# Performance work log

Hardware: AMD Instinct MI355X
Metric: run time of the kernel (lower is better)

The kernel has to match this reference:

```python
import jax, jax.numpy as jnp
import numpy as np

HEAD_DIM = 256
ROTARY_DIM = 128  # max(2, int(0.5*256) rounded down to even)
HALF_ROT = ROTARY_DIM // 2   # 64
HALF_HEAD = HEAD_DIM // 2    # 128
WAVELENGTH = 10000.0
ROPE_SCALING = 1.0
SOFT_CAP = 50.0
EPS = 1e-6
NQ = 8
NKV = 4
GROUPS = NQ // NKV
NEG_INF = -1e9


def rms_norm(x, scale):
    # keras-hub Gemma RMSNorm: fp32 compute, out = x * rsqrt(mean(x^2)+eps) * (1+scale)
    x32 = x.astype(jnp.float32)
    var = jnp.mean(jnp.square(x32), axis=-1, keepdims=True)
    y = x32 * jax.lax.rsqrt(var + EPS)
    return (y * (1.0 + scale.astype(jnp.float32))).astype(x.dtype)


def l2_norm(x):
    # Gemma4VNorm: pure L2 normalization over head_dim, no learned scale
    x32 = x.astype(jnp.float32)
    ss = jnp.sum(jnp.square(x32), axis=-1, keepdims=True)
    return (x32 * jax.lax.rsqrt(ss + EPS)).astype(x.dtype)


def apply_partial_rope(x):
    # x: [B, S, N, HEAD_DIM]. Partial proportional rotation: only the first
    # HALF_ROT elements of each HALF_HEAD half get rotated. RoPE inverse freqs
    # use denominator_dim = HEAD_DIM (not rotary_dim).
    S = x.shape[1]
    inv_freq = 1.0 / (WAVELENGTH ** (jnp.arange(0, ROTARY_DIM, 2, dtype=jnp.float32) / HEAD_DIM))  # [HALF_ROT]
    pos = jnp.arange(S, dtype=jnp.float32) / ROPE_SCALING
    freq = pos[:, None] * inv_freq[None, :]             # [S, HALF_ROT]
    cos = jnp.cos(freq)[None, :, None, :].astype(x.dtype)
    sin = jnp.sin(freq)[None, :, None, :].astype(x.dtype)
    x1 = x[..., :HALF_HEAD]
    x2 = x[..., HALF_HEAD:]
    x1r, x1n = x1[..., :HALF_ROT], x1[..., HALF_ROT:]
    x2r, x2n = x2[..., :HALF_ROT], x2[..., HALF_ROT:]
    # rotate-half form: [x1r, x2r]*cos + [-x2r, x1r]*sin
    y1r = x1r * cos - x2r * sin
    y2r = x2r * cos + x1r * sin
    return jnp.concatenate([y1r, x1n, y2r, x2n], axis=-1)


def setup_inputs() -> dict:
    key = jax.random.key(0)
    ks = jax.random.split(key, 6)
    B, S, D = 2, 2048, 2048
    x = jax.random.normal(ks[0], (B, S, D), jnp.float32)
    # causal mask [B, S, S]
    attention_mask = jnp.broadcast_to(jnp.tril(jnp.ones((S, S), bool))[None], (B, S, S))
    w_scale = 0.02
    Wq = jax.random.normal(ks[1], (NQ, D, HEAD_DIM), jnp.float32) * w_scale
    Wk = jax.random.normal(ks[2], (NKV, D, HEAD_DIM), jnp.float32) * w_scale
    Wv = jax.random.normal(ks[3], (NKV, D, HEAD_DIM), jnp.float32) * w_scale
    Wo = jax.random.normal(ks[4], (NQ, HEAD_DIM, D), jnp.float32) * w_scale
    q_scale = jnp.zeros((HEAD_DIM,), jnp.float32)
    k_scale = jnp.zeros((HEAD_DIM,), jnp.float32)
    return {"x": x, "attention_mask": attention_mask, "Wq": Wq, "Wk": Wk,
            "Wv": Wv, "Wo": Wo, "q_scale": q_scale, "k_scale": k_scale}


def reference(x, attention_mask, Wq, Wk, Wv, Wo, q_scale, k_scale):
    B, S, D = x.shape
    q = jnp.einsum('btd,ndh->btnh', x, Wq)
    q = apply_partial_rope(rms_norm(q, q_scale))
    k = jnp.einsum('bsd,kdh->bskh', x, Wk)
    k = apply_partial_rope(rms_norm(k, k_scale))
    v = l2_norm(jnp.einsum('bsd,kdh->bskh', x, Wv))
    # grouped-query attention, scaling = 1.0 (Gemma4 relies on QK norm)
    qg = q.reshape(B, S, NKV, GROUPS, HEAD_DIM)
    logits = jnp.einsum('btkgh,bskh->bkgts', qg, k)
    # logit soft cap
    logits = jnp.tanh(logits / SOFT_CAP) * SOFT_CAP
    mask = attention_mask[:, None, None, :, :]
    logits = jnp.where(mask, logits, NEG_INF)
    probs = jax.nn.softmax(logits.astype(jnp.float32), axis=-1).astype(logits.dtype)
    out = jnp.einsum('bkgts,bskh->btkgh', probs, v).reshape(B, S, NQ, HEAD_DIM)
    return jnp.einsum('btnh,nhd->btd', out, Wo)
```

## Files before the change

### kernel.cpp

```cpp
#include <hip/hip_runtime.h>

#define AS1 __attribute__((address_space(1)))
#define AS3 __attribute__((address_space(3)))

typedef __attribute__((ext_vector_type(8))) _Float16 f16x8;
typedef __attribute__((ext_vector_type(4))) float f32x4;

__device__ __forceinline__ unsigned short f2h(float f) {
    union { _Float16 h; unsigned short u; } v; v.h = (_Float16)f; return v.u;
}

__device__ __forceinline__ void gload16(const void* g, void* l) {
    __builtin_amdgcn_global_load_lds((const AS1 unsigned int*)g, (AS3 unsigned int*)l, 16, 0, 0);
}

#define GBAR() __builtin_amdgcn_s_barrier()
#define VM4()  asm volatile("s_waitcnt vmcnt(4)" ::: "memory")
#define VM0()  asm volatile("s_waitcnt vmcnt(0)" ::: "memory")

__global__ __launch_bounds__(256) void k_cvt(const float* __restrict__ src,
                                             unsigned short* __restrict__ dst, int n4) {
    int i = blockIdx.x * 256 + threadIdx.x;
    if (i >= n4) return;
    float4 v = ((const float4*)src)[i];
    ushort4 o;
    o.x = f2h(v.x); o.y = f2h(v.y); o.z = f2h(v.z); o.w = f2h(v.w);
    ((ushort4*)dst)[i] = o;
}

__global__ __launch_bounds__(256) void k_transpose_cvt(const float* __restrict__ src,
                                                       unsigned short* __restrict__ dst,
                                                       int ld_src, int ld_dst,
                                                       long zs_src, long zs_dst) {
    __shared__ float tile[32][33];
    long sb = (long)blockIdx.z * zs_src;
    long db = (long)blockIdx.z * zs_dst;
    int c0 = blockIdx.x * 32, r0 = blockIdx.y * 32;
    int tx = threadIdx.x, ty = threadIdx.y;
#pragma unroll
    for (int i = 0; i < 4; i++)
        tile[ty + i * 8][tx] = src[sb + (long)(r0 + ty + i * 8) * ld_src + c0 + tx];
    __syncthreads();
#pragma unroll
    for (int i = 0; i < 4; i++)
        dst[db + (long)(c0 + ty + i * 8) * ld_dst + r0 + tx] = f2h(tile[tx][ty + i * 8]);
}


template<int BUF, int MIH>
__device__ __forceinline__ void rdA(const unsigned short* SA, int wm, int fr, int g,
                                    f16x8 (&af)[4][2]) {
#pragma unroll
    for (int m = 0; m < 4; m++)
#pragma unroll
        for (int kk = 0; kk < 2; kk++) {
            int pos = wm * 64 + m * 16 + fr;
            af[m][kk] = *(const f16x8*)(SA + BUF * 16384 + MIH * 8192 + pos * 64 +
                                        (((kk * 4 + g) ^ (fr & 7)) << 3));
        }
}

template<int BUF, int NIH>
__device__ __forceinline__ void rdB(const unsigned short* SB, int wn, int fr, int g,
                                    f16x8 (&bf)[2][2]) {
#pragma unroll
    for (int ni2 = 0; ni2 < 2; ni2++)
#pragma unroll
        for (int kk = 0; kk < 2; kk++) {
            int pos = wn * 32 + ni2 * 16 + fr;
            bf[ni2][kk] = *(const f16x8*)(SB + BUF * 16384 + NIH * 8192 + pos * 64 +
                                          (((kk * 4 + g) ^ (fr & 7)) << 3));
        }
}

template<int MIH, int NIH>
__device__ __forceinline__ void mm16(f16x8 (&af)[4][2], f16x8 (&bf)[2][2], f32x4 (&acc)[8][4]) {
    __builtin_amdgcn_s_setprio(1);
#pragma unroll
    for (int m = 0; m < 4; m++)
#pragma unroll
        for (int ni2 = 0; ni2 < 2; ni2++)
#pragma unroll
            for (int kk = 0; kk < 2; kk++)
                acc[MIH * 4 + m][NIH * 2 + ni2] = __builtin_amdgcn_mfma_f32_16x16x32_f16(
                    af[m][kk], bf[ni2][kk], acc[MIH * 4 + m][NIH * 2 + ni2], 0, 0, 0);
    __builtin_amdgcn_s_setprio(0);
}

__global__ __launch_bounds__(512, 1) void k_gemm256(const unsigned short* __restrict__ A,
                                                    const unsigned short* __restrict__ Bt,
                                                    float* __restrict__ C,
                                                    int M, int N, int K, int nbx) {
    __shared__ __align__(16) unsigned short sm[65536];
    unsigned short* SA = sm;
    unsigned short* SB = sm + 32768;

    int tid = threadIdx.x, lane = tid & 63, wid = tid >> 6;
    int g = lane >> 4, fr = lane & 15;
    int wm = wid >> 2, wn = wid & 3;

    int bid = blockIdx.x;
    int sid = (bid & 7) * ((int)gridDim.x >> 3) + (bid >> 3);
    int by = sid / nbx, bx = sid % nbx;
    int rowA0 = by * 256, colB0 = bx * 256;

    f32x4 acc[8][4];
#pragma unroll
    for (int mi = 0; mi < 8; mi++)
#pragma unroll
        for (int ni = 0; ni < 4; ni++) acc[mi][ni] = (f32x4){0.f, 0.f, 0.f, 0.f};

    auto stA = [&](int buf, int h, int kt) {
#pragma unroll
        for (int t = 0; t < 2; t++) {
            int i = t * 512 + tid;
            int pos = i >> 3;
            int grow = rowA0 + ((pos >> 6) << 7) + h * 64 + (pos & 63);
            int cg = (i & 7) ^ (pos & 7);
            gload16(A + (size_t)grow * K + kt * 64 + cg * 8,
                    SA + buf * 16384 + h * 8192 + pos * 64 + (i & 7) * 8);
        }
    };
    auto stB = [&](int buf, int h, int kt) {
#pragma unroll
        for (int t = 0; t < 2; t++) {
            int i = t * 512 + tid;
            int pos = i >> 3;
            int gcol = colB0 + ((pos >> 5) << 6) + h * 32 + (pos & 31);
            int cg = (i & 7) ^ (pos & 7);
            gload16(Bt + (size_t)gcol * K + kt * 64 + cg * 8,
                    SB + buf * 16384 + h * 8192 + pos * 64 + (i & 7) * 8);
        }
    };

    int nT = K >> 6;
    stA(0, 0, 0); stB(0, 0, 0); stA(0, 1, 0); stB(0, 1, 0);
    stA(1, 0, 1); stB(1, 0, 1);
    VM4();
    GBAR();

    f16x8 af[4][2], bf[2][2];
    int nIt = nT >> 1;
    for (int it = 0; it < nIt; it++) {
        int T = it * 2;
        bool s36 = (T + 2 < nT), s78 = (T + 3 < nT);
        rdA<0, 0>(SA, wm, fr, g, af); rdB<0, 0>(SB, wn, fr, g, bf);
        stA(1, 1, T + 1);
        GBAR(); mm16<0, 0>(af, bf, acc); GBAR();
        rdB<0, 1>(SB, wn, fr, g, bf);
        stB(1, 1, T + 1);
        GBAR(); mm16<0, 1>(af, bf, acc); GBAR();
        rdA<0, 1>(SA, wm, fr, g, af); rdB<0, 0>(SB, wn, fr, g, bf);
        if (s36) stA(0, 0, T + 2);
        GBAR(); mm16<1, 0>(af, bf, acc); GBAR();
        rdB<0, 1>(SB, wn, fr, g, bf);
        if (s36) { stB(0, 0, T + 2); VM4(); } else { VM0(); }
        GBAR(); mm16<1, 1>(af, bf, acc); GBAR();
        rdA<1, 0>(SA, wm, fr, g, af); rdB<1, 0>(SB, wn, fr, g, bf);
        if (s36) stA(0, 1, T + 2);
        GBAR(); mm16<0, 0>(af, bf, acc); GBAR();
        rdB<1, 1>(SB, wn, fr, g, bf);
        if (s36) stB(0, 1, T + 2);
        GBAR(); mm16<0, 1>(af, bf, acc); GBAR();
        rdA<1, 1>(SA, wm, fr, g, af); rdB<1, 0>(SB, wn, fr, g, bf);
        if (s78) stA(1, 0, T + 3);
        GBAR(); mm16<1, 0>(af, bf, acc); GBAR();
        rdB<1, 1>(SB, wn, fr, g, bf);
        if (s78) { stB(1, 0, T + 3); VM4(); } else { VM0(); }
        GBAR(); mm16<1, 1>(af, bf, acc); GBAR();
    }

#pragma unroll
    for (int mi = 0; mi < 8; mi++) {
        int row = rowA0 + wm * 128 + mi * 16 + g * 4;
#pragma unroll
        for (int ni = 0; ni < 4; ni++) {
            int col = colB0 + wn * 64 + ni * 16 + fr;
#pragma unroll
            for (int r = 0; r < 4; r++)
                C[(size_t)(row + r) * N + col] = acc[mi][ni][r];
        }
    }
}

__global__ __launch_bounds__(256) void k_gemm_f16(const unsigned short* __restrict__ A,
                                                  const unsigned short* __restrict__ Bt,
                                                  float* __restrict__ C,
                                                  int M, int N, int K) {
    __shared__ unsigned short As[128 * 64];
    __shared__ unsigned short Bs[128 * 64];
    int tid = threadIdx.x;
    int lane = tid & 63, wid = tid >> 6;
    int g = lane >> 4, fr = lane & 15;
    int rowA0 = blockIdx.y * 128;
    int colB0 = blockIdx.x * 128;

    f32x4 zero = {0.f, 0.f, 0.f, 0.f};
    f32x4 acc[4][4];
#pragma unroll
    for (int mi = 0; mi < 4; mi++)
#pragma unroll
        for (int ni = 0; ni < 4; ni++) acc[mi][ni] = zero;

    const unsigned short* ag[4];
    const unsigned short* bg[4];
#pragma unroll
    for (int j = 0; j < 4; j++) {
        int id = j * 256 + tid;
        int r = id >> 3;
        int c = (id & 7) ^ (r & 7);
        ag[j] = A + (size_t)(rowA0 + r) * K + c * 8;
        bg[j] = Bt + (size_t)(colB0 + r) * K + c * 8;
    }

    int nK = K >> 6;
    for (int kt = 0; kt < nK; kt++) {
#pragma unroll
        for (int j = 0; j < 4; j++) {
            int id = j * 256 + tid;
            gload16(ag[j], As + id * 8);
            gload16(bg[j], Bs + id * 8);
            ag[j] += 64; bg[j] += 64;
        }
        __syncthreads();
#pragma unroll
        for (int kk = 0; kk < 2; kk++) {
            f16x8 af[4], bfr[4];
#pragma unroll
            for (int mi = 0; mi < 4; mi++) {
                int r = (wid >> 1) * 64 + mi * 16 + fr;
                af[mi] = *(const f16x8*)(As + r * 64 + ((((kk << 2) + g) ^ (r & 7)) << 3));
            }
#pragma unroll
            for (int ni = 0; ni < 4; ni++) {
                int r = (wid & 1) * 64 + ni * 16 + fr;
                bfr[ni] = *(const f16x8*)(Bs + r * 64 + ((((kk << 2) + g) ^ (r & 7)) << 3));
            }
#pragma unroll
            for (int mi = 0; mi < 4; mi++)
#pragma unroll
                for (int ni = 0; ni < 4; ni++)
                    acc[mi][ni] = __builtin_amdgcn_mfma_f32_16x16x32_f16(af[mi], bfr[ni], acc[mi][ni], 0, 0, 0);
        }
        __syncthreads();
    }

#pragma unroll
    for (int mi = 0; mi < 4; mi++) {
        int row = rowA0 + (wid >> 1) * 64 + mi * 16 + g * 4;
#pragma unroll
        for (int ni = 0; ni < 4; ni++) {
            int col = colB0 + (wid & 1) * 64 + ni * 16 + fr;
#pragma unroll
            for (int r = 0; r < 4; r++)
                C[(size_t)(row + r) * N + col] = acc[mi][ni][r];
        }
    }
}

__global__ __launch_bounds__(256) void k_norm_rope(float* __restrict__ qkv,
                                                   const float* __restrict__ q_scale,
                                                   const float* __restrict__ k_scale,
                                                   unsigned short* __restrict__ Qh,
                                                   unsigned short* __restrict__ Kh) {
    __shared__ float Y[256];
    __shared__ float red[4];
    int blk = blockIdx.x;
    int bt = blk >> 4, slot = blk & 15;
    int b = bt >> 11, t = bt & 2047;
    int h = threadIdx.x;
    int lane = h & 63, wid = h >> 6;

    float x = qkv[(size_t)bt * 4096 + slot * 256 + h];
    float v = x * x;
#pragma unroll
    for (int m = 1; m < 64; m <<= 1) v += __shfl_xor(v, m);
    if (lane == 0) red[wid] = v;
    __syncthreads();
    float ss = red[0] + red[1] + red[2] + red[3];

    float y;
    if (slot < 12) {
        float fac = rsqrtf(ss * (1.0f / 256.0f) + 1e-6f);
        const float* sc = (slot < 8) ? q_scale : k_scale;
        y = x * fac * (1.0f + sc[h]);
    } else {
        float fac = rsqrtf(ss + 1e-6f);
        y = x * fac;
    }
    Y[h] = y;
    __syncthreads();

    if (slot < 12) {
        float out;
        int hm = h & 127;
        if (hm < 64) {
            float inv = exp2f(-(float)hm * 0.10381025296522993f);
            float fr = (float)t * inv;
            float s = sinf(fr), c = cosf(fr);
            float y1 = Y[hm], y2 = Y[128 + hm];
            out = (h < 128) ? (y1 * c - y2 * s) : (y2 * c + y1 * s);
        } else {
            out = y;
        }
        unsigned short hv = f2h(out);
        if (slot < 8)
            Qh[((size_t)(b * 8 + slot) * 2048 + t) * 256 + h] = hv;
        else
            Kh[((size_t)(b * 4 + (slot - 8)) * 2048 + t) * 256 + h] = hv;
    } else {
        qkv[(size_t)bt * 4096 + slot * 256 + h] = y;
    }
}

__global__ __launch_bounds__(512, 2) void k_attn(const unsigned short* __restrict__ Qhg,
                                                 const unsigned short* __restrict__ Khg,
                                                 const unsigned short* __restrict__ Vtg,
                                                 unsigned short* __restrict__ attn) {
    __shared__ __align__(16) char smem[140288];
    unsigned short* Ks = (unsigned short*)smem;
    unsigned short* Vs = (unsigned short*)(smem + 65536);
    unsigned short* Ps = (unsigned short*)(smem + 131072);
    float* ML = (float*)(smem + 139264);
    float* X = (float*)smem;

    int id = blockIdx.x;
    int bkv = id & 7;
    int npar = (id >> 3) & 1;
    int pair = id >> 4;
    int b = bkv >> 2, kv = bkv & 3;
    int n = kv * 2 + npar;
    int bn = b * 8 + n;

    int tid = threadIdx.x, lane = tid & 63, wid = tid >> 6;
    int g = lane >> 4, fr = lane & 15;
    int r2 = wid & 3, c2 = wid >> 2;

    const unsigned short* Kh = Khg + (size_t)bkv * 2048 * 256;
    const unsigned short* Vh = Vtg + (size_t)bkv * 256 * 2048;
    const unsigned short* Qb = Qhg + (size_t)bn * 2048 * 256;

    for (int half = 0; half < 2; half++) {
        int j = half ? 31 - pair : pair;
        int q0 = j * 64 + r2 * 16;

        const unsigned short* qrow = Qb + (size_t)(q0 + fr) * 256;
        f16x8 aq[8];
#pragma unroll
        for (int kk = 0; kk < 8; kk++) aq[kk] = *(const f16x8*)(qrow + kk * 32 + g * 8);

        f32x4 zero4 = {0.f, 0.f, 0.f, 0.f};
        f32x4 o[16];
#pragma unroll
        for (int i2 = 0; i2 < 16; i2++) o[i2] = zero4;
        float m_run[4] = {-1e30f, -1e30f, -1e30f, -1e30f};
        float l_run[4] = {0.f, 0.f, 0.f, 0.f};

        auto STAGE = [&](int bufi, int kt2) {
            int k0s = kt2 * 64;
#pragma unroll
            for (int t2 = 0; t2 < 4; t2++) {
                int c_ = t2 * 512 + tid;
                int r = c_ >> 5, c = (c_ & 31) ^ (r & 7);
                gload16(Kh + ((size_t)(k0s + r) * 256 + c * 8), Ks + bufi * 16384 + c_ * 8);
                int d = c_ >> 3, cv = (c_ & 7) ^ (d & 7);
                gload16(Vh + ((size_t)d * 2048 + k0s + cv * 8), Vs + bufi * 16384 + c_ * 8);
            }
        };

        STAGE(0, 0);
        __syncthreads();

        for (int kt = 0; kt <= j; kt++) {
            int cur = kt & 1;
            if (kt < j) STAGE(cur ^ 1, kt + 1);

            const unsigned short* KH = Ks + cur * 16384;
            const unsigned short* VC = Vs + cur * 16384;
            int k0 = kt * 64;

            f32x4 se[2] = {zero4, zero4}, so2[2] = {zero4, zero4};
            __builtin_amdgcn_s_setprio(1);
#pragma unroll
            for (int kk = 0; kk < 8; kk += 2) {
#pragma unroll
                for (int ni = 0; ni < 2; ni++) {
                    int kr = c2 * 32 + ni * 16 + fr;
                    f16x8 bk0 = *(const f16x8*)(KH + kr * 256 + (((kk << 2) + g) ^ (kr & 7)) * 8);
                    f16x8 bk1 = *(const f16x8*)(KH + kr * 256 + ((((kk + 1) << 2) + g) ^ (kr & 7)) * 8);
                    se[ni] = __builtin_amdgcn_mfma_f32_16x16x32_f16(aq[kk], bk0, se[ni], 0, 0, 0);
                    so2[ni] = __builtin_amdgcn_mfma_f32_16x16x32_f16(aq[kk + 1], bk1, so2[ni], 0, 0, 0);
                }
            }
            __builtin_amdgcn_s_setprio(0);

            float p[2][4];
#pragma unroll
            for (int ni = 0; ni < 2; ni++)
#pragma unroll
                for (int r = 0; r < 4; r++) {
                    float s = se[ni][r] + so2[ni][r];
                    float e = __expf(0.04f * s);
                    s = 50.f - 100.f * __builtin_amdgcn_rcpf(1.f + e);
                    int key = k0 + c2 * 32 + ni * 16 + fr;
                    int qr = q0 + g * 4 + r;
                    if (key > qr) s = -1e9f;
                    p[ni][r] = s;
                }

            float mrow[4];
#pragma unroll
            for (int r = 0; r < 4; r++) {
                float m = fmaxf(p[0][r], p[1][r]);
#pragma unroll
                for (int sft = 1; sft < 16; sft <<= 1) m = fmaxf(m, __shfl_xor(m, sft));
                mrow[r] = m;
            }
            int needs = (mrow[0] > m_run[0] + 8.f) || (mrow[1] > m_run[1] + 8.f) ||
                        (mrow[2] > m_run[2] + 8.f) || (mrow[3] > m_run[3] + 8.f);
            if (__any(needs)) {
                float sw[4];
#pragma unroll
                for (int r = 0; r < 4; r++) {
                    float mnew = fmaxf(m_run[r], mrow[r]);
                    sw[r] = __expf(m_run[r] - mnew);
                    m_run[r] = mnew;
                    l_run[r] *= sw[r];
                }
#pragma unroll
                for (int nt = 0; nt < 16; nt++)
#pragma unroll
                    for (int r = 0; r < 4; r++) o[nt][r] *= sw[r];
            }
#pragma unroll
            for (int r = 0; r < 4; r++) {
                float p0 = __expf(p[0][r] - m_run[r]); p[0][r] = p0;
                float p1 = __expf(p[1][r] - m_run[r]); p[1][r] = p1;
                l_run[r] += p0 + p1;
            }

            unsigned short* Pw = Ps + wid * 512;
#pragma unroll
            for (int ni = 0; ni < 2; ni++)
#pragma unroll
                for (int r = 0; r < 4; r++) {
                    int q = g * 4 + r, kl = ni * 16 + fr;
                    Pw[q * 32 + (((kl >> 3) ^ (q & 3)) << 3) + (kl & 7)] = f2h(p[ni][r]);
                }
            f16x8 ap = *(const f16x8*)(Pw + fr * 32 + ((g ^ (fr & 3)) << 3));

            __builtin_amdgcn_s_setprio(1);
#pragma unroll
            for (int nt = 0; nt < 16; nt++) {
                int dr = nt * 16 + fr;
                f16x8 bv = *(const f16x8*)(VC + dr * 64 + ((((c2 << 2) + g) ^ (dr & 7)) << 3));
                o[nt] = __builtin_amdgcn_mfma_f32_16x16x32_f16(ap, bv, o[nt], 0, 0, 0);
            }
            __builtin_amdgcn_s_setprio(0);
            __syncthreads();
        }

#pragma unroll
        for (int r = 0; r < 4; r++) {
            float l = l_run[r];
#pragma unroll
            for (int sft = 1; sft < 16; sft <<= 1) l += __shfl_xor(l, sft);
            l_run[r] = l;
        }

        int mlbase = ((c2 * 4 + r2) * 4 + g) * 4;
        if (fr == 0) {
#pragma unroll
            for (int r = 0; r < 4; r++) {
                ML[(mlbase + r) * 2] = m_run[r];
                ML[(mlbase + r) * 2 + 1] = l_run[r];
            }
        }
        __syncthreads();
        int plbase = (((1 - c2) * 4 + r2) * 4 + g) * 4;
        float wS[4], linv[4];
#pragma unroll
        for (int r = 0; r < 4; r++) {
            float mp = ML[(plbase + r) * 2], lp = ML[(plbase + r) * 2 + 1];
            float ms = fmaxf(m_run[r], mp);
            wS[r] = __expf(m_run[r] - ms);
            float wp = __expf(mp - ms);
            linv[r] = __builtin_amdgcn_rcpf(l_run[r] * wS[r] + lp * wp);
        }
        float* Xl = X + (r2 * 64 + lane) * 68;
        if (c2 == 1) {
#pragma unroll
            for (int nt = 0; nt < 16; nt++)
#pragma unroll
                for (int r = 0; r < 4; r++) Xl[nt * 4 + r] = o[nt][r] * wS[r];
        }
        __syncthreads();
        if (c2 == 0) {
#pragma unroll
            for (int nt = 0; nt < 16; nt++)
#pragma unroll
                for (int r = 0; r < 4; r++) {
                    float val = (o[nt][r] * wS[r] + Xl[nt * 4 + r]) * linv[r];
                    int qr = q0 + g * 4 + r;
                    attn[(size_t)(b * 2048 + qr) * 2048 + n * 256 + nt * 16 + fr] = f2h(val);
                }
        }
        __syncthreads();
    }
}

extern "C" void kernel_launch(void* const* d_in, const int* in_sizes, int n_in,
                              void* d_out, int out_size, void* d_ws, size_t ws_size,
                              hipStream_t stream) {
    const float* x       = (const float*)d_in[0];
    const float* Wq      = (const float*)d_in[2];
    const float* Wk      = (const float*)d_in[3];
    const float* Wv      = (const float*)d_in[4];
    const float* Wo      = (const float*)d_in[5];
    const float* q_scale = (const float*)d_in[6];
    const float* k_scale = (const float*)d_in[7];
    float* out = (float*)d_out;
    char* ws = (char*)d_ws;

    const size_t MB = 1024 * 1024;
    unsigned short* xh    = (unsigned short*)ws;
    unsigned short* Qh    = (unsigned short*)ws;
    unsigned short* WT    = (unsigned short*)(ws + 16 * MB);
    unsigned short* Kh    = (unsigned short*)(ws + 16 * MB);
    unsigned short* Vt    = (unsigned short*)(ws + 24 * MB);
    unsigned short* WoT   = (unsigned short*)(ws + 32 * MB);
    float*          qkv   = (float*)(ws + 40 * MB);
    unsigned short* attnb = (unsigned short*)(ws + 40 * MB);

    dim3 tb(32, 8);
    k_cvt<<<dim3(8192), dim3(256), 0, stream>>>(x, xh, 2097152);
    k_transpose_cvt<<<dim3(8, 64, 8), tb, 0, stream>>>(Wq, WT, 256, 2048, 524288L, 524288L);
    k_transpose_cvt<<<dim3(8, 64, 4), tb, 0, stream>>>(Wk, WT + (size_t)2048 * 2048, 256, 2048, 524288L, 524288L);
    k_transpose_cvt<<<dim3(8, 64, 4), tb, 0, stream>>>(Wv, WT + (size_t)3072 * 2048, 256, 2048, 524288L, 524288L);

    k_gemm256<<<dim3(256), dim3(512), 0, stream>>>(xh, WT, qkv, 4096, 4096, 2048, 16);
    k_norm_rope<<<dim3(65536), dim3(256), 0, stream>>>(qkv, q_scale, k_scale, Qh, Kh);
    for (int b = 0; b < 2; b++)
        k_transpose_cvt<<<dim3(8, 64, 4), tb, 0, stream>>>(qkv + (size_t)b * 2048 * 4096 + 3072,
                                                           Vt + (size_t)b * 4 * 256 * 2048,
                                                           4096, 2048, 256L, 524288L);
    k_attn<<<dim3(256), dim3(512), 0, stream>>>(Qh, Kh, Vt, attnb);

    k_transpose_cvt<<<dim3(64, 64, 1), tb, 0, stream>>>(Wo, WoT, 2048, 2048, 0L, 0L);
    k_gemm_f16<<<dim3(16, 32), dim3(256), 0, stream>>>(attnb, WoT, out, 4096, 2048, 2048);
}
```

Baseline: 275.4 us.

## Compute transposed S in attention to feed P to PV MFMA from registers

Measured after the change: 274.9 us. Within noise of the previous version (-0.2%).

```diff
diff --git a/kernel.cpp b/kernel.cpp
--- a/kernel.cpp
+++ b/kernel.cpp
@@ -4,7 +4,10 @@
 #define AS3 __attribute__((address_space(3)))
 
 typedef __attribute__((ext_vector_type(8))) _Float16 f16x8;
+typedef __attribute__((ext_vector_type(4))) _Float16 f16x4;
 typedef __attribute__((ext_vector_type(4))) float f32x4;
+
+#define MFMA_K16(a, b, c) __builtin_amdgcn_mfma_f32_16x16x16f16(a, b, c, 0, 0, 0)
 
 __device__ __forceinline__ unsigned short f2h(float f) {
     union { _Float16 h; unsigned short u; } v; v.h = (_Float16)f; return v.u;
@@ -45,7 +48,6 @@
     for (int i = 0; i < 4; i++)
         dst[db + (long)(c0 + ty + i * 8) * ld_dst + r0 + tx] = f2h(tile[tx][ty + i * 8]);
 }
-
 
 template<int BUF, int MIH>
 __device__ __forceinline__ void rdA(const unsigned short* SA, int wm, int fr, int g,
@@ -317,11 +319,10 @@
                                                  const unsigned short* __restrict__ Khg,
                                                  const unsigned short* __restrict__ Vtg,
                                                  unsigned short* __restrict__ attn) {
-    __shared__ __align__(16) char smem[140288];
+    __shared__ __align__(16) char smem[132096];
     unsigned short* Ks = (unsigned short*)smem;
     unsigned short* Vs = (unsigned short*)(smem + 65536);
-    unsigned short* Ps = (unsigned short*)(smem + 131072);
-    float* ML = (float*)(smem + 139264);
+    float* ML = (float*)(smem + 131072);
     float* X = (float*)smem;
 
     int id = blockIdx.x;
@@ -335,11 +336,33 @@
     int tid = threadIdx.x, lane = tid & 63, wid = tid >> 6;
     int g = lane >> 4, fr = lane & 15;
     int r2 = wid & 3, c2 = wid >> 2;
+    int g4 = g * 4;
 
     const unsigned short* Kh = Khg + (size_t)bkv * 2048 * 256;
     const unsigned short* Vh = Vtg + (size_t)bkv * 256 * 2048;
     const unsigned short* Qb = Qhg + (size_t)bn * 2048 * 256;
 
+    const unsigned short* kb[4];
+    const unsigned short* vb[4];
+    int sdst[4];
+#pragma unroll
+    for (int t2 = 0; t2 < 4; t2++) {
+        int c_ = t2 * 512 + tid;
+        int r = c_ >> 5, c = (c_ & 31) ^ (r & 7);
+        kb[t2] = Kh + (size_t)r * 256 + c * 8;
+        int d = c_ >> 3, cv = (c_ & 7) ^ (d & 7);
+        vb[t2] = Vh + (size_t)d * 2048 + cv * 8;
+        sdst[t2] = c_ * 8;
+    }
+
+    int krbase[2];
+#pragma unroll
+    for (int t16 = 0; t16 < 2; t16++) krbase[t16] = (c2 * 32 + t16 * 16 + fr) * 256;
+    int s7 = fr & 7;
+    int vslot[2];
+#pragma unroll
+    for (int t16 = 0; t16 < 2; t16++) vslot[t16] = (((c2 * 4 + t16 * 2 + (g >> 1)) ^ s7) << 3) + (g & 1) * 4;
+
     for (int half = 0; half < 2; half++) {
         int j = half ? 31 - pair : pair;
         int q0 = j * 64 + r2 * 16;
@@ -353,18 +376,14 @@
         f32x4 o[16];
 #pragma unroll
         for (int i2 = 0; i2 < 16; i2++) o[i2] = zero4;
-        float m_run[4] = {-1e30f, -1e30f, -1e30f, -1e30f};
-        float l_run[4] = {0.f, 0.f, 0.f, 0.f};
+        float m_run = -1e30f;
+        float l_run = 0.f;
 
         auto STAGE = [&](int bufi, int kt2) {
-            int k0s = kt2 * 64;
 #pragma unroll
             for (int t2 = 0; t2 < 4; t2++) {
-                int c_ = t2 * 512 + tid;
-                int r = c_ >> 5, c = (c_ & 31) ^ (r & 7);
-                gload16(Kh + ((size_t)(k0s + r) * 256 + c * 8), Ks + bufi * 16384 + c_ * 8);
-                int d = c_ >> 3, cv = (c_ & 7) ^ (d & 7);
-                gload16(Vh + ((size_t)d * 2048 + k0s + cv * 8), Vs + bufi * 16384 + c_ * 8);
+                gload16(kb[t2] + (size_t)kt2 * 16384, Ks + bufi * 16384 + sdst[t2]);
+                gload16(vb[t2] + kt2 * 64, Vs + bufi * 16384 + sdst[t2]);
             }
         };
 
@@ -384,115 +403,95 @@
 #pragma unroll
             for (int kk = 0; kk < 8; kk += 2) {
 #pragma unroll
-                for (int ni = 0; ni < 2; ni++) {
-                    int kr = c2 * 32 + ni * 16 + fr;
-                    f16x8 bk0 = *(const f16x8*)(KH + kr * 256 + (((kk << 2) + g) ^ (kr & 7)) * 8);
-                    f16x8 bk1 = *(const f16x8*)(KH + kr * 256 + ((((kk + 1) << 2) + g) ^ (kr & 7)) * 8);
-                    se[ni] = __builtin_amdgcn_mfma_f32_16x16x32_f16(aq[kk], bk0, se[ni], 0, 0, 0);
-                    so2[ni] = __builtin_amdgcn_mfma_f32_16x16x32_f16(aq[kk + 1], bk1, so2[ni], 0, 0, 0);
+                for (int t16 = 0; t16 < 2; t16++) {
+                    f16x8 bk0 = *(const f16x8*)(KH + krbase[t16] + ((((kk << 2) + g) ^ s7) << 3));
+                    f16x8 bk1 = *(const f16x8*)(KH + krbase[t16] + (((((kk + 1) << 2) + g) ^ s7) << 3));
+                    se[t16] = __builtin_amdgcn_mfma_f32_16x16x32_f16(bk0, aq[kk], se[t16], 0, 0, 0);
+                    so2[t16] = __builtin_amdgcn_mfma_f32_16x16x32_f16(bk1, aq[kk + 1], so2[t16], 0, 0, 0);
                 }
             }
             __builtin_amdgcn_s_setprio(0);
 
-            float p[2][4];
-#pragma unroll
-            for (int ni = 0; ni < 2; ni++)
+            int qg = q0 + fr;
+            float pv[2][4];
+            float ml = -1e30f;
+#pragma unroll
+            for (int t16 = 0; t16 < 2; t16++)
 #pragma unroll
                 for (int r = 0; r < 4; r++) {
-                    float s = se[ni][r] + so2[ni][r];
+                    float s = se[t16][r] + so2[t16][r];
                     float e = __expf(0.04f * s);
                     s = 50.f - 100.f * __builtin_amdgcn_rcpf(1.f + e);
-                    int key = k0 + c2 * 32 + ni * 16 + fr;
-                    int qr = q0 + g * 4 + r;
-                    if (key > qr) s = -1e9f;
-                    p[ni][r] = s;
+                    int key = k0 + c2 * 32 + t16 * 16 + g4 + r;
+                    if (key > qg) s = -1e9f;
+                    pv[t16][r] = s;
+                    ml = fmaxf(ml, s);
                 }
-
-            float mrow[4];
-#pragma unroll
-            for (int r = 0; r < 4; r++) {
-                float m = fmaxf(p[0][r], p[1][r]);
-#pragma unroll
-                for (int sft = 1; sft < 16; sft <<= 1) m = fmaxf(m, __shfl_xor(m, sft));
-                mrow[r] = m;
+            ml = fmaxf(ml, __shfl_xor(ml, 16));
+            ml = fmaxf(ml, __shfl_xor(ml, 32));
+
+            if (__any(ml > m_run + 8.f)) {
+                float mnew = fmaxf(m_run, ml);
+                float swl = __expf(m_run - mnew);
+                m_run = mnew;
+                l_run *= swl;
+                float swr[4];
+#pragma unroll
+                for (int r = 0; r < 4; r++) swr[r] = __shfl(swl, g4 + r);
+#pragma unroll
+                for (int nt = 0; nt < 16; nt++)
+#pragma unroll
+                    for (int r = 0; r < 4; r++) o[nt][r] *= swr[r];
             }
-            int needs = (mrow[0] > m_run[0] + 8.f) || (mrow[1] > m_run[1] + 8.f) ||
-                        (mrow[2] > m_run[2] + 8.f) || (mrow[3] > m_run[3] + 8.f);
-            if (__any(needs)) {
-                float sw[4];
+
+            f16x4 pf[2];
+#pragma unroll
+            for (int t16 = 0; t16 < 2; t16++)
 #pragma unroll
                 for (int r = 0; r < 4; r++) {
-                    float mnew = fmaxf(m_run[r], mrow[r]);
-                    sw[r] = __expf(m_run[r] - mnew);
-                    m_run[r] = mnew;
-                    l_run[r] *= sw[r];
+                    float p = __expf(pv[t16][r] - m_run);
+                    l_run += p;
+                    pf[t16][r] = (_Float16)p;
                 }
-#pragma unroll
-                for (int nt = 0; nt < 16; nt++)
-#pragma unroll
-                    for (int r = 0; r < 4; r++) o[nt][r] *= sw[r];
-            }
-#pragma unroll
-            for (int r = 0; r < 4; r++) {
-                float p0 = __expf(p[0][r] - m_run[r]); p[0][r] = p0;
-                float p1 = __expf(p[1][r] - m_run[r]); p[1][r] = p1;
-                l_run[r] += p0 + p1;
-            }
-
-            unsigned short* Pw = Ps + wid * 512;
-#pragma unroll
-            for (int ni = 0; ni < 2; ni++)
-#pragma unroll
-                for (int r = 0; r < 4; r++) {
-                    int q = g * 4 + r, kl = ni * 16 + fr;
-                    Pw[q * 32 + (((kl >> 3) ^ (q & 3)) << 3) + (kl & 7)] = f2h(p[ni][r]);
-                }
-            f16x8 ap = *(const f16x8*)(Pw + fr * 32 + ((g ^ (fr & 3)) << 3));
 
             __builtin_amdgcn_s_setprio(1);
 #pragma unroll
             for (int nt = 0; nt < 16; nt++) {
-                int dr = nt * 16 + fr;
-                f16x8 bv = *(const f16x8*)(VC + dr * 64 + ((((c2 << 2) + g) ^ (dr & 7)) << 3));
-                o[nt] = __builtin_amdgcn_mfma_f32_16x16x32_f16(ap, bv, o[nt], 0, 0, 0);
+                int dbase = (nt * 16 + fr) * 64;
+                f16x4 bv0 = *(const f16x4*)(VC + dbase + vslot[0]);
+                f16x4 bv1 = *(const f16x4*)(VC + dbase + vslot[1]);
+                o[nt] = MFMA_K16(pf[0], bv0, o[nt]);
+                o[nt] = MFMA_K16(pf[1], bv1, o[nt]);
             }
             __builtin_amdgcn_s_setprio(0);
             __syncthreads();
         }
 
+        float l2 = l_run + __shfl_xor(l_run, 16);
+        l2 += __shfl_xor(l2, 32);
+        if (lane < 16) {
+            float* mlw = ML + ((c2 * 4 + r2) * 16 + lane) * 2;
+            mlw[0] = m_run; mlw[1] = l2;
+        }
+        __syncthreads();
+        float wO[4], li[4];
 #pragma unroll
         for (int r = 0; r < 4; r++) {
-            float l = l_run[r];
-#pragma unroll
-            for (int sft = 1; sft < 16; sft <<= 1) l += __shfl_xor(l, sft);
-            l_run[r] = l;
-        }
-
-        int mlbase = ((c2 * 4 + r2) * 4 + g) * 4;
-        if (fr == 0) {
-#pragma unroll
-            for (int r = 0; r < 4; r++) {
-                ML[(mlbase + r) * 2] = m_run[r];
-                ML[(mlbase + r) * 2 + 1] = l_run[r];
-            }
-        }
-        __syncthreads();
-        int plbase = (((1 - c2) * 4 + r2) * 4 + g) * 4;
-        float wS[4], linv[4];
-#pragma unroll
-        for (int r = 0; r < 4; r++) {
-            float mp = ML[(plbase + r) * 2], lp = ML[(plbase + r) * 2 + 1];
-            float ms = fmaxf(m_run[r], mp);
-            wS[r] = __expf(m_run[r] - ms);
-            float wp = __expf(mp - ms);
-            linv[r] = __builtin_amdgcn_rcpf(l_run[r] * wS[r] + lp * wp);
+            int qq = g4 + r;
+            const float* p0 = ML + (r2 * 16 + qq) * 2;
+            const float* p1 = ML + ((4 + r2) * 16 + qq) * 2;
+            float m0 = p0[0], l0 = p0[1], m1 = p1[0], l1 = p1[1];
+            float ms = fmaxf(m0, m1);
+            float w0 = __expf(m0 - ms), w1 = __expf(m1 - ms);
+            li[r] = __builtin_amdgcn_rcpf(fmaxf(l0 * w0 + l1 * w1, 1e-30f));
+            wO[r] = c2 ? w1 : w0;
         }
         float* Xl = X + (r2 * 64 + lane) * 68;
         if (c2 == 1) {
 #pragma unroll
             for (int nt = 0; nt < 16; nt++)
 #pragma unroll
-                for (int r = 0; r < 4; r++) Xl[nt * 4 + r] = o[nt][r] * wS[r];
+                for (int r = 0; r < 4; r++) Xl[nt * 4 + r] = o[nt][r] * wO[r];
         }
         __syncthreads();
         if (c2 == 0) {
@@ -500,8 +499,8 @@
             for (int nt = 0; nt < 16; nt++)
 #pragma unroll
                 for (int r = 0; r < 4; r++) {
-                    float val = (o[nt][r] * wS[r] + Xl[nt * 4 + r]) * linv[r];
-                    int qr = q0 + g * 4 + r;
+                    float val = (o[nt][r] * wO[r] + Xl[nt * 4 + r]) * li[r];
+                    int qr = q0 + g4 + r;
                     attn[(size_t)(b * 2048 + qr) * 2048 + n * 256 + nt * 16 + fr] = f2h(val);
                 }
         }
```
